# Optimization experiments

Measured on AMD Instinct MI355X. Metric: run time of the kernel, lower is better.

Reference implementation:

```python
import jax, jax.numpy as jnp
import numpy as np
import math

INF = 1e12  # constant.INFINITY_NUMBER in the original repo


def setup_inputs() -> dict:
    key = jax.random.key(0)
    ks = jax.random.split(key, 12)
    B, S, W, D = 16, 512, 8, 768
    M, Wm = 2, 64
    U, Wu = 32, 16
    V = 32000
    words = jax.random.randint(ks[0], (B, S, W), 0, V)
    masks = jax.random.randint(ks[1], (B, S, W), 0, 2).astype(bool)
    main = jax.random.randint(ks[2], (B, M, Wm), 0, V)
    main_mask = jax.random.randint(ks[3], (B, M, Wm), 0, 2).astype(bool)
    user = jax.random.randint(ks[4], (B, U, Wu), 0, V)
    user_mask = jax.random.randint(ks[5], (B, U, Wu), 0, 2).astype(bool)
    # sparse-ish dependency adjacency
    adj = (jax.random.uniform(ks[6], (B, S, S)) < 0.05).astype(jnp.float32)
    emb_weight = jax.random.normal(ks[7], (V, D), jnp.float32) * 0.02
    K_w = jax.random.normal(ks[8], (D, D), jnp.float32) * (1.0 / math.sqrt(D))
    K_b = jnp.zeros((D,), jnp.float32)
    Q_w = jax.random.normal(ks[9], (D, D), jnp.float32) * (1.0 / math.sqrt(D))
    Q_b = jnp.zeros((D,), jnp.float32)
    return {"words": words, "masks": masks, "main": main, "main_mask": main_mask,
            "user": user, "user_mask": user_mask, "adj": adj,
            "emb_weight": emb_weight, "K_w": K_w, "K_b": K_b, "Q_w": Q_w, "Q_b": Q_b}


def _masked_max(embs, mask, axis):
    # masked_fill(mask, -INF) -> max(axis) ; caller fixes residual -INF rows
    return jnp.max(jnp.where(mask[..., None], -INF, embs), axis=axis)


def reference(words, masks, main, main_mask, user, user_mask, adj,
              emb_weight, K_w, K_b, Q_w, Q_b):
    D = emb_weight.shape[1]

    word_embs = emb_weight[words]   # [B,S,W,D]
    main_embs = emb_weight[main]    # [B,M,Wm,D]
    user_embs = emb_weight[user]    # [B,U,Wu,D]

    # node mask from adjacency: True where node has no in/out edges
    mask = ((adj.sum(axis=2) + adj.sum(axis=1)) == 0)[:, :, None]  # [B,S,1]

    # main: masked max-pool over word pieces, zero fully-masked rows
    main_e = _masked_max(main_embs, main_mask, axis=2)             # [B,M,D]
    main_e = jnp.where(main_e == -INF, 0.0, main_e)

    # user: masked max-pool over word pieces then over users
    user_e = _masked_max(user_embs, user_mask, axis=2)             # [B,U,D]
    user_e = jnp.max(user_e, axis=1)                               # [B,D]
    user_e = jnp.where(user_e == -INF, 0.0, user_e)

    # token embeddings: masked max-pool over word pieces (no -INF fix in original)
    g = _masked_max(word_embs, masks, axis=2)                      # [B,S,D]

    # single-head attention: softmax(K g (Q g)^T / sqrt(D)) @ g
    key_ = g @ K_w.T + K_b                                         # [B,S,D]
    query = g @ Q_w.T + Q_b                                        # [B,S,D]
    scores = jnp.einsum('bsd,btd->bst', key_, query) / math.sqrt(D)
    dense_graph = jax.nn.softmax(scores, axis=2)                   # [B,S,S]
    gcn_out = jnp.einsum('bst,btd->bsd', dense_graph, g)           # [B,S,D]

    adj_sm = jax.nn.softmax(adj, axis=2)

    return (gcn_out, mask, dense_graph, adj_sm,
            jnp.squeeze(main_e), jnp.squeeze(user_e))
```

## Files before the change

kernel.cpp:

```cpp
#include <hip/hip_runtime.h>
#include <hip/hip_bf16.h>
#include <math.h>

static constexpr int Bn = 16, Sn = 512, Wn = 8, Dn = 768;
static constexpr int Mn_ = 2, WMn = 64;
static constexpr int Un = 32, WUn = 16;

#define INF_VAL 1e12f
#define INV_SQRT_D 0.03608439182435161f

static constexpr size_t OFF_GCN   = 0;
static constexpr size_t OFF_MASK  = 6291456;
static constexpr size_t OFF_DENSE = 6299648;
static constexpr size_t OFF_ADJ   = 10493952;
static constexpr size_t OFF_MAIN  = 14688256;
static constexpr size_t OFF_USER  = 14712832;

static constexpr size_t WSB_GBF     = 0;
static constexpr size_t WSB_GT      = 12582912;
static constexpr size_t WSB_DENSEBF = 25165824;
static constexpr size_t WSB_PARTU   = 33554432;
static constexpr size_t WSB_PARTM   = 35127296;
static constexpr size_t WSB_BCAT    = 35520512;
static constexpr size_t WSB_KBAR    = 35526656;
static constexpr size_t WSB_QBAR    = 35532800;
static constexpr size_t WSB_U       = 35538944;
static constexpr size_t WSB_V       = 35545088;
static constexpr size_t WSB_CONSTS  = 35551232;
static constexpr size_t WSB_QS      = 35551296;
static constexpr size_t WSB_KQ      = 35584064;
static constexpr size_t WSB_COLSUM  = 35616832;
static constexpr size_t WSB_FLAGS   = 35649600;
static constexpr size_t WSB_ROWSUM  = 35682368;
static constexpr size_t WSB_UVU     = 35715136;
static constexpr size_t WSB_UVV     = 35764288;

typedef __attribute__((ext_vector_type(8))) short short8;
typedef __attribute__((ext_vector_type(4))) float f32x4;

static __device__ __forceinline__ ushort f2bf(float f) {
    union { float f; unsigned u; } v; v.f = f;
    unsigned u = v.u;
    unsigned r = (u + 0x7FFFu + ((u >> 16) & 1u)) >> 16;
    return (ushort)r;
}

static __device__ __forceinline__ void gload16(const void* g, void* lds) {
    __builtin_amdgcn_global_load_lds(
        (const __attribute__((address_space(1))) void*)g,
        (__attribute__((address_space(3))) void*)lds, 16, 0, 0);
}

static __device__ __forceinline__ void fmax4(float4& a, const float4& x) {
    a.x = fmaxf(a.x, x.x); a.y = fmaxf(a.y, x.y);
    a.z = fmaxf(a.z, x.z); a.w = fmaxf(a.w, x.w);
}

__global__ __launch_bounds__(256)
void fold1(const float* __restrict__ K_w, const float* __restrict__ K_b,
           const float* __restrict__ Q_w, const float* __restrict__ Q_b,
           double* __restrict__ kbar, double* __restrict__ qbar,
           ushort* __restrict__ Kwb, ushort* __restrict__ Qwb,
           float* __restrict__ bcat, float* __restrict__ colsum) {
    int blk = blockIdx.x, t = threadIdx.x;
    if (blk < 192) {
        int wv = t >> 6, lane = t & 63;
        int r = blk * 4 + wv;
        double sk = 0.0, sq = 0.0;
        for (int d = lane; d < Dn; d += 64) {
            sk += (double)K_w[(size_t)r * Dn + d];
            sq += (double)Q_w[(size_t)r * Dn + d];
        }
        #pragma unroll
        for (int off = 32; off > 0; off >>= 1) {
            sk += __shfl_down(sk, off, 64);
            sq += __shfl_down(sq, off, 64);
        }
        if (lane == 0) {
            kbar[r] = -1e12 * sk + (double)K_b[r];
            qbar[r] = -1e12 * sq + (double)Q_b[r];
        }
    } else if (blk < 254) {
        const int NV = Dn * Dn / 4;
        for (int i = (blk - 192) * 256 + t; i < 2 * NV; i += 62 * 256) {
            float4 x; ushort4 o;
            if (i < NV) x = ((const float4*)K_w)[i];
            else        x = ((const float4*)Q_w)[i - NV];
            o.x = f2bf(x.x); o.y = f2bf(x.y); o.z = f2bf(x.z); o.w = f2bf(x.w);
            if (i < NV) ((ushort4*)Kwb)[i] = o;
            else        ((ushort4*)Qwb)[i - NV] = o;
        }
    } else if (blk == 254) {
        for (int i = t; i < 1536; i += 256)
            bcat[i] = (i < Dn) ? K_b[i] : Q_b[i - Dn];
    } else {
        for (int i = t; i < Bn * Sn; i += 256) colsum[i] = 0.f;
    }
}

__global__ __launch_bounds__(64)
void uv_part(const float* __restrict__ K_w, const float* __restrict__ Q_w,
             const double* __restrict__ kbar, const double* __restrict__ qbar,
             double* __restrict__ uvu, double* __restrict__ uvv) {
    int j = blockIdx.x * 64 + threadIdx.x;
    int e0 = blockIdx.y * 96;
    double su = 0.0, sv = 0.0;
    for (int e = e0; e < e0 + 96; ++e) {
        su += (double)K_w[(size_t)e * Dn + j] * qbar[e];
        sv += (double)Q_w[(size_t)e * Dn + j] * kbar[e];
    }
    uvu[(size_t)blockIdx.y * Dn + j] = su;
    uvv[(size_t)blockIdx.y * Dn + j] = sv;
}

__global__ __launch_bounds__(64)
void uvred_consts(const double* __restrict__ uvu, const double* __restrict__ uvv,
                  const double* __restrict__ kbar, const double* __restrict__ qbar,
                  const float* __restrict__ K_b, const float* __restrict__ Q_b,
                  double* __restrict__ u, double* __restrict__ v,
                  double* __restrict__ consts) {
    int blk = blockIdx.x;
    int l = threadIdx.x;
    if (blk < 12) {
        int j = blk * 64 + l;
        double su = 0.0, sv = 0.0;
        #pragma unroll
        for (int c = 0; c < 8; ++c) {
            su += uvu[(size_t)c * Dn + j];
            sv += uvv[(size_t)c * Dn + j];
        }
        u[j] = su; v[j] = sv;
    } else {
        double c0 = 0.0, c1 = 0.0, c2 = 0.0;
        for (int e = l; e < Dn; e += 64) {
            c0 += kbar[e] * (double)Q_b[e];
            c1 += kbar[e] * qbar[e];
            c2 += qbar[e] * (double)K_b[e];
        }
        #pragma unroll
        for (int off = 32; off > 0; off >>= 1) {
            c0 += __shfl_down(c0, off, 64);
            c1 += __shfl_down(c1, off, 64);
            c2 += __shfl_down(c2, off, 64);
        }
        if (l == 0) { consts[0] = c0; consts[1] = c1; consts[2] = c2; }
    }
}

__global__ __launch_bounds__(512)
void adjsm_colsum_kernel(const float* __restrict__ adj, float* __restrict__ adjsm,
                         float* __restrict__ colsum, float* __restrict__ rowsum) {
    int blk = blockIdx.x;
    int b = blk >> 5, rc = blk & 31;
    int t = threadIdx.x;
    const float* base = adj + ((size_t)b * Sn + rc * 16) * Sn;
    float* obase = adjsm + ((size_t)b * Sn + rc * 16) * Sn;
    const float EM1 = 0.36787944117144233f;
    const float EP1 = 2.718281828459045f;
    __shared__ float red[8];
    float colacc = 0.f;
    for (int r = 0; r < 16; ++r) {
        float a = base[(size_t)r * Sn + t];
        colacc += a;
        float s = a;
        #pragma unroll
        for (int off = 32; off > 0; off >>= 1) s += __shfl_down(s, off, 64);
        if ((t & 63) == 0) red[t >> 6] = s;
        __syncthreads();
        float n1 = red[0] + red[1] + red[2] + red[3]
                 + red[4] + red[5] + red[6] + red[7];
        float e1, e0;
        if (n1 > 0.f) { e1 = 1.f; e0 = EM1; } else { e1 = EP1; e0 = 1.f; }
        float denom = n1 * e1 + (512.f - n1) * e0;
        float inv = 1.f / denom;
        obase[(size_t)r * Sn + t] = (a == 1.f ? e1 : e0) * inv;
        if (t == 0) rowsum[(size_t)b * Sn + rc * 16 + r] = n1;
        __syncthreads();
    }
    atomicAdd(&colsum[(size_t)b * Sn + t], colacc);
}

__global__ __launch_bounds__(192)
void pool_g_kernel(const int* __restrict__ words, const int* __restrict__ masks,
                   const float* __restrict__ emb,
                   const double* __restrict__ u, const double* __restrict__ v,
                   const double* __restrict__ consts,
                   ushort* __restrict__ gbf, float* __restrict__ qs,
                   float* __restrict__ kq, int* __restrict__ flags) {
    int bs = blockIdx.x;
    int t = threadIdx.x;
    const int* wrow = words + (size_t)bs * Wn;
    const int* mrow = masks + (size_t)bs * Wn;
    float4 acc = make_float4(-INF_VAL, -INF_VAL, -INF_VAL, -INF_VAL);
    int nm = 0;
    #pragma unroll
    for (int w = 0; w < Wn; ++w) {
        int mk = mrow[w];
        nm += (mk != 0);
        if (mk != 0) continue;
        float4 x = ((const float4*)(emb + (size_t)wrow[w] * Dn))[t];
        fmax4(acc, x);
    }
    ushort4 o;
    o.x = f2bf(acc.x); o.y = f2bf(acc.y); o.z = f2bf(acc.z); o.w = f2bf(acc.w);
    ((ushort4*)(gbf + (size_t)bs * Dn))[t] = o;
    int j = t * 4;
    double dv = v[j] * (double)acc.x + v[j+1] * (double)acc.y
              + v[j+2] * (double)acc.z + v[j+3] * (double)acc.w;
    double du = u[j] * (double)acc.x + u[j+1] * (double)acc.y
              + u[j+2] * (double)acc.z + u[j+3] * (double)acc.w;
    #pragma unroll
    for (int off = 32; off > 0; off >>= 1) {
        dv += __shfl_down(dv, off, 64);
        du += __shfl_down(du, off, 64);
    }
    __shared__ double rr[6];
    if ((t & 63) == 0) { rr[t >> 6] = dv; rr[3 + (t >> 6)] = du; }
    __syncthreads();
    if (t == 0) {
        qs[bs] = (float)(rr[0] + rr[1] + rr[2] + consts[0]);
        kq[bs] = (float)(rr[3] + rr[4] + rr[5] + consts[2]);
        flags[bs] = (nm == Wn) ? 1 : 0;
    }
}

__global__ __launch_bounds__(192)
void pool_s1(const int* __restrict__ main_idx, const int* __restrict__ mmask,
             const int* __restrict__ user_idx, const int* __restrict__ umask,
             const float* __restrict__ emb,
             float* __restrict__ partM, float* __restrict__ partU) {
    int blk = blockIdx.x;
    int t = threadIdx.x;
    const int *irow, *mrow;
    float* dst;
    if (blk < 128) {
        int bm = blk >> 2, ch = blk & 3;
        irow = main_idx + (size_t)bm * WMn + ch * 16;
        mrow = mmask + (size_t)bm * WMn + ch * 16;
        dst = partM + (size_t)blk * Dn;
    } else {
        int bu = blk - 128;
        irow = user_idx + (size_t)bu * WUn;
        mrow = umask + (size_t)bu * WUn;
        dst = partU + (size_t)bu * Dn;
    }
    float4 acc = make_float4(-INF_VAL, -INF_VAL, -INF_VAL, -INF_VAL);
    #pragma unroll
    for (int w = 0; w < 16; ++w) {
        if (mrow[w] != 0) continue;
        float4 x = ((const float4*)(emb + (size_t)irow[w] * Dn))[t];
        fmax4(acc, x);
    }
    ((float4*)dst)[t] = acc;
}

__global__ __launch_bounds__(192)
void pool_s2m(const float* __restrict__ partM, const float* __restrict__ partU,
              float* __restrict__ outM, float* __restrict__ outU,
              const float* __restrict__ rowsum, const float* __restrict__ colsum,
              float* __restrict__ maskout) {
    int blk = blockIdx.x;
    int t = threadIdx.x;
    if (blk >= 48) {
        int i = (blk - 48) * 192 + t;
        if (i < Bn * Sn)
            maskout[i] = ((rowsum[i] + colsum[i]) == 0.f) ? 1.f : 0.f;
        return;
    }
    float4 acc = make_float4(-INF_VAL, -INF_VAL, -INF_VAL, -INF_VAL);
    float* dst;
    if (blk < 32) {
        #pragma unroll
        for (int c = 0; c < 4; ++c) {
            float4 x = ((const float4*)(partM + (size_t)(blk * 4 + c) * Dn))[t];
            fmax4(acc, x);
        }
        dst = outM + (size_t)blk * Dn;
    } else {
        int b = blk - 32;
        for (int u2 = 0; u2 < Un; ++u2) {
            float4 x = ((const float4*)(partU + (size_t)(b * Un + u2) * Dn))[t];
            fmax4(acc, x);
        }
        dst = outU + (size_t)b * Dn;
    }
    if (acc.x == -INF_VAL) acc.x = 0.f;
    if (acc.y == -INF_VAL) acc.y = 0.f;
    if (acc.z == -INF_VAL) acc.z = 0.f;
    if (acc.w == -INF_VAL) acc.w = 0.f;
    ((float4*)dst)[t] = acc;
}

__global__ __launch_bounds__(256)
void transpose_g(const ushort* __restrict__ gbf, ushort* __restrict__ gT) {
    __shared__ ushort tile[32][33];
    int b = blockIdx.z;
    int d0 = blockIdx.x * 32, s0 = blockIdx.y * 32;
    int tx = threadIdx.x & 31, ty = threadIdx.x >> 5;
    #pragma unroll
    for (int i = 0; i < 4; ++i)
        tile[ty + i * 8][tx] = gbf[((size_t)(b * Sn + s0 + ty + i * 8)) * Dn + d0 + tx];
    __syncthreads();
    #pragma unroll
    for (int i = 0; i < 4; ++i)
        gT[((size_t)(b * Dn + d0 + ty + i * 8)) * Sn + s0 + tx] = tile[tx][ty + i * 8];
}

template<int OUT_BF16, int HASBIAS, int SPLITC>
__global__ __launch_bounds__(256)
void gemm_mfma(const ushort* __restrict__ A, const ushort* __restrict__ B,
               const float* __restrict__ bias, void* __restrict__ Cout,
               void* __restrict__ Cout2,
               int Km, int lda, int ldb, int ldc,
               long long sA, long long sB, long long sC) {
    __shared__ ushort As[128 * 64];
    __shared__ ushort Bs[128 * 64];
    const ushort* Ab = A + (size_t)blockIdx.z * sA;
    const ushort* Bb = B + (size_t)blockIdx.z * sB;
    int i0 = blockIdx.y * 128, j0 = blockIdx.x * 128;
    int tid = threadIdx.x;
    int lane = tid & 63, wv = tid >> 6;
    int wr = wv >> 1, wc = wv & 1;
    int ln15 = lane & 15, lkg = lane >> 4;
    int sub = lane >> 3;
    int c8  = lane & 7;

    f32x4 acc[4][4] = {};

    for (int k0 = 0; k0 < Km; k0 += 64) {
        #pragma unroll
        for (int it = 0; it < 4; ++it) {
            int r = it * 32 + wv * 8 + sub;
            int cc = c8 ^ (r & 7);
            ushort* dstA = As + (it * 4096 + wv * 1024) / 2;
            ushort* dstB = Bs + (it * 4096 + wv * 1024) / 2;
            gload16(Ab + (size_t)(i0 + r) * lda + k0 + cc * 8, dstA);
            gload16(Bb + (size_t)(j0 + r) * ldb + k0 + cc * 8, dstB);
        }
        __syncthreads();
        #pragma unroll
        for (int kh = 0; kh < 2; ++kh) {
            short8 af[4], bfr[4];
            int kc = kh * 4 + lkg;
            #pragma unroll
            for (int f = 0; f < 4; ++f) {
                int ra = wr * 64 + f * 16 + ln15;
                af[f] = *(const short8*)((const char*)As + ra * 128 + ((kc ^ (ra & 7)) << 4));
                int rb = wc * 64 + f * 16 + ln15;
                bfr[f] = *(const short8*)((const char*)Bs + rb * 128 + ((kc ^ (rb & 7)) << 4));
            }
            #pragma unroll
            for (int fa = 0; fa < 4; ++fa)
                #pragma unroll
                for (int fb = 0; fb < 4; ++fb)
                    acc[fa][fb] = __builtin_amdgcn_mfma_f32_16x16x32_bf16(
                        af[fa], bfr[fb], acc[fa][fb], 0, 0, 0);
        }
        __syncthreads();
    }

    #pragma unroll
    for (int fa = 0; fa < 4; ++fa) {
        #pragma unroll
        for (int fb = 0; fb < 4; ++fb) {
            int n = j0 + wc * 64 + fb * 16 + ln15;
            float bv = HASBIAS ? bias[n] : 0.0f;
            #pragma unroll
            for (int rr = 0; rr < 4; ++rr) {
                int m = i0 + wr * 64 + fa * 16 + lkg * 4 + rr;
                float val = acc[fa][fb][rr] + bv;
                if (SPLITC) {
                    ushort* dst = (n < Dn) ? (ushort*)Cout : (ushort*)Cout2;
                    int nn = (n < Dn) ? n : n - Dn;
                    dst[(size_t)m * ldc + nn] = f2bf(val);
                } else if (OUT_BF16) {
                    ((ushort*)Cout)[(size_t)blockIdx.z * sC + (size_t)m * ldc + n] = f2bf(val);
                } else {
                    ((float*)Cout)[(size_t)blockIdx.z * sC + (size_t)m * ldc + n] = val;
                }
            }
        }
    }
}

__global__ __launch_bounds__(256)
void softmax_fix(float* __restrict__ dense, const int* __restrict__ flags,
                 const float* __restrict__ qs, const float* __restrict__ kq,
                 const double* __restrict__ consts, ushort* __restrict__ densebf) {
    int bs = blockIdx.x;
    int b = bs >> 9;
    int t = threadIdx.x;
    float* row = dense + (size_t)bs * 512;
    int f0 = flags[(b << 9) + t];
    int f1 = flags[(b << 9) + t + 256];
    bool sm = flags[bs] != 0;
    float x0, x1;
    if (sm) {
        float c1i = (float)consts[1] * INV_SQRT_D;
        x0 = f0 ? c1i : qs[(b << 9) + t] * INV_SQRT_D;
        x1 = f1 ? c1i : qs[(b << 9) + t + 256] * INV_SQRT_D;
    } else {
        float kqi = kq[bs] * INV_SQRT_D;
        x0 = f0 ? kqi : row[t] * INV_SQRT_D;
        x1 = f1 ? kqi : row[t + 256] * INV_SQRT_D;
    }
    float m = fmaxf(x0, x1);
    #pragma unroll
    for (int off = 32; off > 0; off >>= 1) m = fmaxf(m, __shfl_down(m, off, 64));
    __shared__ float red[4];
    __shared__ float bmax, bsum;
    if ((t & 63) == 0) red[t >> 6] = m;
    __syncthreads();
    if (t == 0) bmax = fmaxf(fmaxf(red[0], red[1]), fmaxf(red[2], red[3]));
    __syncthreads();
    float mx = bmax;
    float e0 = expf(x0 - mx), e1 = expf(x1 - mx);
    float s = e0 + e1;
    #pragma unroll
    for (int off = 32; off > 0; off >>= 1) s += __shfl_down(s, off, 64);
    if ((t & 63) == 0) red[t >> 6] = s;
    __syncthreads();
    if (t == 0) bsum = red[0] + red[1] + red[2] + red[3];
    __syncthreads();
    float inv = 1.f / bsum;
    float p0 = e0 * inv, p1 = e1 * inv;
    row[t] = p0; row[t + 256] = p1;
    ushort* bro = densebf + (size_t)bs * 512;
    bro[t] = f2bf(p0); bro[t + 256] = f2bf(p1);
}

extern "C" void kernel_launch(void* const* d_in, const int* in_sizes, int n_in,
                              void* d_out, int out_size, void* d_ws, size_t ws_size,
                              hipStream_t stream) {
    const int*   words     = (const int*)d_in[0];
    const int*   masks     = (const int*)d_in[1];
    const int*   main_idx  = (const int*)d_in[2];
    const int*   main_mask = (const int*)d_in[3];
    const int*   user_idx  = (const int*)d_in[4];
    const int*   user_mask = (const int*)d_in[5];
    const float* adj       = (const float*)d_in[6];
    const float* emb       = (const float*)d_in[7];
    const float* K_w       = (const float*)d_in[8];
    const float* K_b       = (const float*)d_in[9];
    const float* Q_w       = (const float*)d_in[10];
    const float* Q_b       = (const float*)d_in[11];

    float* out = (float*)d_out;
    char*  ws8 = (char*)d_ws;

    ushort* gbf     = (ushort*)(ws8 + WSB_GBF);
    ushort* gT      = (ushort*)(ws8 + WSB_GT);
    ushort* densebf = (ushort*)(ws8 + WSB_DENSEBF);
    float*  partU   = (float*)(ws8 + WSB_PARTU);
    float*  partM   = (float*)(ws8 + WSB_PARTM);
    float*  bcat    = (float*)(ws8 + WSB_BCAT);
    double* kbar    = (double*)(ws8 + WSB_KBAR);
    double* qbar    = (double*)(ws8 + WSB_QBAR);
    double* u       = (double*)(ws8 + WSB_U);
    double* v       = (double*)(ws8 + WSB_V);
    double* consts  = (double*)(ws8 + WSB_CONSTS);
    float*  qs      = (float*)(ws8 + WSB_QS);
    float*  kq      = (float*)(ws8 + WSB_KQ);
    float*  colsum  = (float*)(ws8 + WSB_COLSUM);
    int*    flags   = (int*)(ws8 + WSB_FLAGS);
    float*  rowsum  = (float*)(ws8 + WSB_ROWSUM);
    double* uvu     = (double*)(ws8 + WSB_UVU);
    double* uvv     = (double*)(ws8 + WSB_UVV);

    ushort* Kwb     = (ushort*)(out + OFF_DENSE);
    ushort* Qwb     = Kwb + (size_t)Dn * Dn;
    ushort* keybf   = (ushort*)(out + OFF_GCN);
    ushort* querybf = keybf + (size_t)Bn * Sn * Dn;
    float*  dense   = out + OFF_DENSE;

    fold1<<<256, 256, 0, stream>>>(K_w, K_b, Q_w, Q_b, kbar, qbar, Kwb, Qwb, bcat, colsum);
    uv_part<<<dim3(Dn / 64, 8), 64, 0, stream>>>(K_w, Q_w, kbar, qbar, uvu, uvv);
    uvred_consts<<<13, 64, 0, stream>>>(uvu, uvv, kbar, qbar, K_b, Q_b, u, v, consts);

    adjsm_colsum_kernel<<<Bn * 32, 512, 0, stream>>>(adj, out + OFF_ADJ, colsum, rowsum);

    pool_g_kernel<<<Bn * Sn, 192, 0, stream>>>(words, masks, emb, u, v, consts,
                                               gbf, qs, kq, flags);
    pool_s1<<<640, 192, 0, stream>>>(main_idx, main_mask, user_idx, user_mask,
                                     emb, partM, partU);
    pool_s2m<<<91, 192, 0, stream>>>(partM, partU, out + OFF_MAIN, out + OFF_USER,
                                     rowsum, colsum, out + OFF_MASK);

    transpose_g<<<dim3(Dn / 32, Sn / 32, Bn), 256, 0, stream>>>(gbf, gT);

    gemm_mfma<1, 1, 1><<<dim3(2 * Dn / 128, (Bn * Sn) / 128, 1), 256, 0, stream>>>(
        gbf, Kwb, bcat, keybf, querybf, Dn, Dn, Dn, Dn, 0, 0, 0);

    gemm_mfma<0, 0, 0><<<dim3(Sn / 128, Sn / 128, Bn), 256, 0, stream>>>(
        keybf, querybf, nullptr, dense, nullptr, Dn, Dn, Dn, Sn,
        (long long)Sn * Dn, (long long)Sn * Dn, (long long)Sn * Sn);

    softmax_fix<<<Bn * Sn, 256, 0, stream>>>(dense, flags, qs, kq, consts, densebf);

    gemm_mfma<0, 0, 0><<<dim3(Dn / 128, Sn / 128, Bn), 256, 0, stream>>>(
        densebf, gT, nullptr, out + OFF_GCN, nullptr, Sn, Sn, Sn, Dn,
        (long long)Sn * Sn, (long long)Dn * Sn, (long long)Sn * Dn);
}
```

Measured before the change: 170.4 us.

## Fold K and Q projections into a single precomputed D×D matrix

The attention scores are reassociated as g·(K_wᵀQ_w)·gᵀ. A D×D product matrix Mt is computed once, then a single GEMM g·Mt gives h. The previous path used two projection GEMMs producing key and query. Bias cross-terms become per-row and per-column scalar corrections (ga, gb, consts[3]) that the softmax kernel adds. This halves the projection GEMM work, at the cost of an extra small weight transpose and GEMM, and bf16 rounding of the folded matrix may shift numerics.

```diff
diff --git a/kernel.cpp b/kernel.cpp
--- a/kernel.cpp
+++ b/kernel.cpp
@@ -19,21 +19,30 @@
 static constexpr size_t WSB_GBF     = 0;
 static constexpr size_t WSB_GT      = 12582912;
 static constexpr size_t WSB_DENSEBF = 25165824;
-static constexpr size_t WSB_PARTU   = 33554432;
-static constexpr size_t WSB_PARTM   = 35127296;
-static constexpr size_t WSB_BCAT    = 35520512;
-static constexpr size_t WSB_KBAR    = 35526656;
-static constexpr size_t WSB_QBAR    = 35532800;
-static constexpr size_t WSB_U       = 35538944;
-static constexpr size_t WSB_V       = 35545088;
-static constexpr size_t WSB_CONSTS  = 35551232;
-static constexpr size_t WSB_QS      = 35551296;
-static constexpr size_t WSB_KQ      = 35584064;
-static constexpr size_t WSB_COLSUM  = 35616832;
-static constexpr size_t WSB_FLAGS   = 35649600;
-static constexpr size_t WSB_ROWSUM  = 35682368;
-static constexpr size_t WSB_UVU     = 35715136;
-static constexpr size_t WSB_UVV     = 35764288;
+static constexpr size_t WSB_HBF     = 33554432;
+static constexpr size_t WSB_KWT     = 46137344;
+static constexpr size_t WSB_QWT     = 47316992;
+static constexpr size_t WSB_MT      = 48496640;
+static constexpr size_t WSB_PARTU   = 49676288;
+static constexpr size_t WSB_PARTM   = 51249152;
+static constexpr size_t WSB_KBAR    = 51642368;
+static constexpr size_t WSB_QBAR    = 51648512;
+static constexpr size_t WSB_U       = 51654656;
+static constexpr size_t WSB_V       = 51660800;
+static constexpr size_t WSB_VA      = 51666944;
+static constexpr size_t WSB_VB      = 51673088;
+static constexpr size_t WSB_CONSTS  = 51679232;
+static constexpr size_t WSB_QS      = 51679296;
+static constexpr size_t WSB_KQ      = 51712064;
+static constexpr size_t WSB_GA      = 51744832;
+static constexpr size_t WSB_GB      = 51777600;
+static constexpr size_t WSB_COLSUM  = 51810368;
+static constexpr size_t WSB_FLAGS   = 51843136;
+static constexpr size_t WSB_ROWSUM  = 51875904;
+static constexpr size_t WSB_UVU     = 51908672;
+static constexpr size_t WSB_UVV     = 51957824;
+static constexpr size_t WSB_UVA     = 52006976;
+static constexpr size_t WSB_UVB     = 52056128;
 
 typedef __attribute__((ext_vector_type(8))) short short8;
 typedef __attribute__((ext_vector_type(4))) float f32x4;
@@ -60,8 +69,8 @@
 void fold1(const float* __restrict__ K_w, const float* __restrict__ K_b,
            const float* __restrict__ Q_w, const float* __restrict__ Q_b,
            double* __restrict__ kbar, double* __restrict__ qbar,
-           ushort* __restrict__ Kwb, ushort* __restrict__ Qwb,
-           float* __restrict__ bcat, float* __restrict__ colsum) {
+           ushort* __restrict__ KwbT, ushort* __restrict__ QwbT,
+           float* __restrict__ colsum) {
     int blk = blockIdx.x, t = threadIdx.x;
     if (blk < 192) {
         int wv = t >> 6, lane = t & 63;
@@ -80,19 +89,21 @@
             kbar[r] = -1e12 * sk + (double)K_b[r];
             qbar[r] = -1e12 * sq + (double)Q_b[r];
         }
-    } else if (blk < 254) {
-        const int NV = Dn * Dn / 4;
-        for (int i = (blk - 192) * 256 + t; i < 2 * NV; i += 62 * 256) {
-            float4 x; ushort4 o;
-            if (i < NV) x = ((const float4*)K_w)[i];
-            else        x = ((const float4*)Q_w)[i - NV];
-            o.x = f2bf(x.x); o.y = f2bf(x.y); o.z = f2bf(x.z); o.w = f2bf(x.w);
-            if (i < NV) ((ushort4*)Kwb)[i] = o;
-            else        ((ushort4*)Qwb)[i - NV] = o;
-        }
-    } else if (blk == 254) {
-        for (int i = t; i < 1536; i += 256)
-            bcat[i] = (i < Dn) ? K_b[i] : Q_b[i - Dn];
+    } else if (blk < 1344) {
+        int tt = blk - 192;
+        const float* src = (tt < 576) ? K_w : Q_w;
+        ushort* dst = (tt < 576) ? KwbT : QwbT;
+        int t6 = (tt < 576) ? tt : tt - 576;
+        int e0 = (t6 % 24) * 32, i0 = (t6 / 24) * 32;
+        __shared__ ushort tile[32][33];
+        int tx = t & 31, ty = t >> 5;
+        #pragma unroll
+        for (int i2 = 0; i2 < 4; ++i2)
+            tile[ty + i2 * 8][tx] = f2bf(src[(size_t)(e0 + ty + i2 * 8) * Dn + i0 + tx]);
+        __syncthreads();
+        #pragma unroll
+        for (int i2 = 0; i2 < 4; ++i2)
+            dst[(size_t)(i0 + ty + i2 * 8) * Dn + e0 + tx] = tile[tx][ty + i2 * 8];
     } else {
         for (int i = t; i < Bn * Sn; i += 256) colsum[i] = 0.f;
     }
@@ -100,50 +111,64 @@
 
 __global__ __launch_bounds__(64)
 void uv_part(const float* __restrict__ K_w, const float* __restrict__ Q_w,
+             const float* __restrict__ K_b, const float* __restrict__ Q_b,
              const double* __restrict__ kbar, const double* __restrict__ qbar,
-             double* __restrict__ uvu, double* __restrict__ uvv) {
+             double* __restrict__ uvu, double* __restrict__ uvv,
+             double* __restrict__ uva, double* __restrict__ uvb) {
     int j = blockIdx.x * 64 + threadIdx.x;
     int e0 = blockIdx.y * 96;
-    double su = 0.0, sv = 0.0;
+    double su = 0.0, sv = 0.0, sa = 0.0, sb = 0.0;
     for (int e = e0; e < e0 + 96; ++e) {
-        su += (double)K_w[(size_t)e * Dn + j] * qbar[e];
-        sv += (double)Q_w[(size_t)e * Dn + j] * kbar[e];
+        double kw = (double)K_w[(size_t)e * Dn + j];
+        double qw = (double)Q_w[(size_t)e * Dn + j];
+        su += kw * qbar[e];
+        sv += qw * kbar[e];
+        sa += kw * (double)Q_b[e];
+        sb += qw * (double)K_b[e];
     }
     uvu[(size_t)blockIdx.y * Dn + j] = su;
     uvv[(size_t)blockIdx.y * Dn + j] = sv;
+    uva[(size_t)blockIdx.y * Dn + j] = sa;
+    uvb[(size_t)blockIdx.y * Dn + j] = sb;
 }
 
 __global__ __launch_bounds__(64)
 void uvred_consts(const double* __restrict__ uvu, const double* __restrict__ uvv,
+                  const double* __restrict__ uva, const double* __restrict__ uvb,
                   const double* __restrict__ kbar, const double* __restrict__ qbar,
                   const float* __restrict__ K_b, const float* __restrict__ Q_b,
                   double* __restrict__ u, double* __restrict__ v,
+                  double* __restrict__ va, double* __restrict__ vb,
                   double* __restrict__ consts) {
     int blk = blockIdx.x;
     int l = threadIdx.x;
     if (blk < 12) {
         int j = blk * 64 + l;
-        double su = 0.0, sv = 0.0;
+        double su = 0.0, sv = 0.0, sa = 0.0, sb = 0.0;
         #pragma unroll
         for (int c = 0; c < 8; ++c) {
             su += uvu[(size_t)c * Dn + j];
             sv += uvv[(size_t)c * Dn + j];
-        }
-        u[j] = su; v[j] = sv;
+            sa += uva[(size_t)c * Dn + j];
+            sb += uvb[(size_t)c * Dn + j];
+        }
+        u[j] = su; v[j] = sv; va[j] = sa; vb[j] = sb;
     } else {
-        double c0 = 0.0, c1 = 0.0, c2 = 0.0;
+        double c0 = 0.0, c1 = 0.0, c2 = 0.0, c3 = 0.0;
         for (int e = l; e < Dn; e += 64) {
             c0 += kbar[e] * (double)Q_b[e];
             c1 += kbar[e] * qbar[e];
             c2 += qbar[e] * (double)K_b[e];
+            c3 += (double)K_b[e] * (double)Q_b[e];
         }
         #pragma unroll
         for (int off = 32; off > 0; off >>= 1) {
             c0 += __shfl_down(c0, off, 64);
             c1 += __shfl_down(c1, off, 64);
             c2 += __shfl_down(c2, off, 64);
-        }
-        if (l == 0) { consts[0] = c0; consts[1] = c1; consts[2] = c2; }
+            c3 += __shfl_down(c3, off, 64);
+        }
+        if (l == 0) { consts[0] = c0; consts[1] = c1; consts[2] = c2; consts[3] = c3; }
     }
 }
 
@@ -184,9 +209,11 @@
 void pool_g_kernel(const int* __restrict__ words, const int* __restrict__ masks,
                    const float* __restrict__ emb,
                    const double* __restrict__ u, const double* __restrict__ v,
+                   const double* __restrict__ va, const double* __restrict__ vb,
                    const double* __restrict__ consts,
                    ushort* __restrict__ gbf, float* __restrict__ qs,
-                   float* __restrict__ kq, int* __restrict__ flags) {
+                   float* __restrict__ kq, float* __restrict__ ga,
+                   float* __restrict__ gb, int* __restrict__ flags) {
     int bs = blockIdx.x;
     int t = threadIdx.x;
     const int* wrow = words + (size_t)bs * Wn;
@@ -209,17 +236,28 @@
               + v[j+2] * (double)acc.z + v[j+3] * (double)acc.w;
     double du = u[j] * (double)acc.x + u[j+1] * (double)acc.y
               + u[j+2] * (double)acc.z + u[j+3] * (double)acc.w;
+    double da = va[j] * (double)acc.x + va[j+1] * (double)acc.y
+              + va[j+2] * (double)acc.z + va[j+3] * (double)acc.w;
+    double db = vb[j] * (double)acc.x + vb[j+1] * (double)acc.y
+              + vb[j+2] * (double)acc.z + vb[j+3] * (double)acc.w;
     #pragma unroll
     for (int off = 32; off > 0; off >>= 1) {
         dv += __shfl_down(dv, off, 64);
         du += __shfl_down(du, off, 64);
-    }
-    __shared__ double rr[6];
-    if ((t & 63) == 0) { rr[t >> 6] = dv; rr[3 + (t >> 6)] = du; }
+        da += __shfl_down(da, off, 64);
+        db += __shfl_down(db, off, 64);
+    }
+    __shared__ double rr[12];
+    if ((t & 63) == 0) {
+        rr[t >> 6] = dv; rr[3 + (t >> 6)] = du;
+        rr[6 + (t >> 6)] = da; rr[9 + (t >> 6)] = db;
+    }
     __syncthreads();
     if (t == 0) {
         qs[bs] = (float)(rr[0] + rr[1] + rr[2] + consts[0]);
         kq[bs] = (float)(rr[3] + rr[4] + rr[5] + consts[2]);
+        ga[bs] = (float)(rr[6] + rr[7] + rr[8]);
+        gb[bs] = (float)(rr[9] + rr[10] + rr[11]);
         flags[bs] = (nm == Wn) ? 1 : 0;
     }
 }
@@ -306,11 +344,10 @@
         gT[((size_t)(b * Dn + d0 + ty + i * 8)) * Sn + s0 + tx] = tile[tx][ty + i * 8];
 }
 
-template<int OUT_BF16, int HASBIAS, int SPLITC>
+template<int OUT_BF16>
 __global__ __launch_bounds__(256)
 void gemm_mfma(const ushort* __restrict__ A, const ushort* __restrict__ B,
-               const float* __restrict__ bias, void* __restrict__ Cout,
-               void* __restrict__ Cout2,
+               void* __restrict__ Cout,
                int Km, int lda, int ldb, int ldc,
                long long sA, long long sB, long long sC) {
     __shared__ ushort As[128 * 64];
@@ -364,16 +401,11 @@
         #pragma unroll
         for (int fb = 0; fb < 4; ++fb) {
             int n = j0 + wc * 64 + fb * 16 + ln15;
-            float bv = HASBIAS ? bias[n] : 0.0f;
             #pragma unroll
             for (int rr = 0; rr < 4; ++rr) {
                 int m = i0 + wr * 64 + fa * 16 + lkg * 4 + rr;
-                float val = acc[fa][fb][rr] + bv;
-                if (SPLITC) {
-                    ushort* dst = (n < Dn) ? (ushort*)Cout : (ushort*)Cout2;
-                    int nn = (n < Dn) ? n : n - Dn;
-                    dst[(size_t)m * ldc + nn] = f2bf(val);
-                } else if (OUT_BF16) {
+                float val = acc[fa][fb][rr];
+                if (OUT_BF16) {
                     ((ushort*)Cout)[(size_t)blockIdx.z * sC + (size_t)m * ldc + n] = f2bf(val);
                 } else {
                     ((float*)Cout)[(size_t)blockIdx.z * sC + (size_t)m * ldc + n] = val;
@@ -386,6 +418,7 @@
 __global__ __launch_bounds__(256)
 void softmax_fix(float* __restrict__ dense, const int* __restrict__ flags,
                  const float* __restrict__ qs, const float* __restrict__ kq,
+                 const float* __restrict__ ga, const float* __restrict__ gb,
                  const double* __restrict__ consts, ushort* __restrict__ densebf) {
     int bs = blockIdx.x;
     int b = bs >> 9;
@@ -401,8 +434,9 @@
         x1 = f1 ? c1i : qs[(b << 9) + t + 256] * INV_SQRT_D;
     } else {
         float kqi = kq[bs] * INV_SQRT_D;
-        x0 = f0 ? kqi : row[t] * INV_SQRT_D;
-        x1 = f1 ? kqi : row[t + 256] * INV_SQRT_D;
+        float corr = ga[bs] + (float)consts[3];
+        x0 = f0 ? kqi : (row[t] + corr + gb[(b << 9) + t]) * INV_SQRT_D;
+        x1 = f1 ? kqi : (row[t + 256] + corr + gb[(b << 9) + t + 256]) * INV_SQRT_D;
     }
     float m = fmaxf(x0, x1);
     #pragma unroll
@@ -451,36 +485,46 @@
     ushort* gbf     = (ushort*)(ws8 + WSB_GBF);
     ushort* gT      = (ushort*)(ws8 + WSB_GT);
     ushort* densebf = (ushort*)(ws8 + WSB_DENSEBF);
+    ushort* hbf     = (ushort*)(ws8 + WSB_HBF);
+    ushort* KwbT    = (ushort*)(ws8 + WSB_KWT);
+    ushort* QwbT    = (ushort*)(ws8 + WSB_QWT);
+    ushort* Mt      = (ushort*)(ws8 + WSB_MT);
     float*  partU   = (float*)(ws8 + WSB_PARTU);
     float*  partM   = (float*)(ws8 + WSB_PARTM);
-    float*  bcat    = (float*)(ws8 + WSB_BCAT);
     double* kbar    = (double*)(ws8 + WSB_KBAR);
     double* qbar    = (double*)(ws8 + WSB_QBAR);
     double* u       = (double*)(ws8 + WSB_U);
     double* v       = (double*)(ws8 + WSB_V);
+    double* va      = (double*)(ws8 + WSB_VA);
+    double* vb      = (double*)(ws8 + WSB_VB);
     double* consts  = (double*)(ws8 + WSB_CONSTS);
     float*  qs      = (float*)(ws8 + WSB_QS);
     float*  kq      = (float*)(ws8 + WSB_KQ);
+    float*  ga      = (float*)(ws8 + WSB_GA);
+    float*  gb      = (float*)(ws8 + WSB_GB);
     float*  colsum  = (float*)(ws8 + WSB_COLSUM);
     int*    flags   = (int*)(ws8 + WSB_FLAGS);
     float*  rowsum  = (float*)(ws8 + WSB_ROWSUM);
     double* uvu     = (double*)(ws8 + WSB_UVU);
     double* uvv     = (double*)(ws8 + WSB_UVV);
-
-    ushort* Kwb     = (ushort*)(out + OFF_DENSE);
-    ushort* Qwb     = Kwb + (size_t)Dn * Dn;
-    ushort* keybf   = (ushort*)(out + OFF_GCN);
-    ushort* querybf = keybf + (size_t)Bn * Sn * Dn;
-    float*  dense   = out + OFF_DENSE;
-
-    fold1<<<256, 256, 0, stream>>>(K_w, K_b, Q_w, Q_b, kbar, qbar, Kwb, Qwb, bcat, colsum);
-    uv_part<<<dim3(Dn / 64, 8), 64, 0, stream>>>(K_w, Q_w, kbar, qbar, uvu, uvv);
-    uvred_consts<<<13, 64, 0, stream>>>(uvu, uvv, kbar, qbar, K_b, Q_b, u, v, consts);
+    double* uva     = (double*)(ws8 + WSB_UVA);
+    double* uvb     = (double*)(ws8 + WSB_UVB);
+
+    float* dense = out + OFF_DENSE;
+
+    fold1<<<1345, 256, 0, stream>>>(K_w, K_b, Q_w, Q_b, kbar, qbar, KwbT, QwbT, colsum);
+    uv_part<<<dim3(Dn / 64, 8), 64, 0, stream>>>(K_w, Q_w, K_b, Q_b, kbar, qbar,
+                                                 uvu, uvv, uva, uvb);
+    uvred_consts<<<13, 64, 0, stream>>>(uvu, uvv, uva, uvb, kbar, qbar, K_b, Q_b,
+                                        u, v, va, vb, consts);
+
+    gemm_mfma<1><<<dim3(6, 6, 1), 256, 0, stream>>>(
+        QwbT, KwbT, Mt, Dn, Dn, Dn, Dn, 0, 0, 0);
 
     adjsm_colsum_kernel<<<Bn * 32, 512, 0, stream>>>(adj, out + OFF_ADJ, colsum, rowsum);
 
-    pool_g_kernel<<<Bn * Sn, 192, 0, stream>>>(words, masks, emb, u, v, consts,
-                                               gbf, qs, kq, flags);
+    pool_g_kernel<<<Bn * Sn, 192, 0, stream>>>(words, masks, emb, u, v, va, vb, consts,
+                                               gbf, qs, kq, ga, gb, flags);
     pool_s1<<<640, 192, 0, stream>>>(main_idx, main_mask, user_idx, user_mask,
                                      emb, partM, partU);
     pool_s2m<<<91, 192, 0, stream>>>(partM, partU, out + OFF_MAIN, out + OFF_USER,
@@ -488,16 +532,16 @@
 
     transpose_g<<<dim3(Dn / 32, Sn / 32, Bn), 256, 0, stream>>>(gbf, gT);
 
-    gemm_mfma<1, 1, 1><<<dim3(2 * Dn / 128, (Bn * Sn) / 128, 1), 256, 0, stream>>>(
-        gbf, Kwb, bcat, keybf, querybf, Dn, Dn, Dn, Dn, 0, 0, 0);
-
-    gemm_mfma<0, 0, 0><<<dim3(Sn / 128, Sn / 128, Bn), 256, 0, stream>>>(
-        keybf, querybf, nullptr, dense, nullptr, Dn, Dn, Dn, Sn,
+    gemm_mfma<1><<<dim3(6, 64, 1), 256, 0, stream>>>(
+        gbf, Mt, hbf, Dn, Dn, Dn, Dn, 0, 0, 0);
+
+    gemm_mfma<0><<<dim3(4, 4, Bn), 256, 0, stream>>>(
+        hbf, gbf, dense, Dn, Dn, Dn, Sn,
         (long long)Sn * Dn, (long long)Sn * Dn, (long long)Sn * Sn);
 
-    softmax_fix<<<Bn * Sn, 256, 0, stream>>>(dense, flags, qs, kq, consts, densebf);
-
-    gemm_mfma<0, 0, 0><<<dim3(Dn / 128, Sn / 128, Bn), 256, 0, stream>>>(
-        densebf, gT, nullptr, out + OFF_GCN, nullptr, Sn, Sn, Sn, Dn,
+    softmax_fix<<<Bn * Sn, 256, 0, stream>>>(dense, flags, qs, kq, ga, gb, consts, densebf);
+
+    gemm_mfma<0><<<dim3(6, 4, Bn), 256, 0, stream>>>(
+        densebf, gT, out + OFF_GCN, Sn, Sn, Sn, Dn,
         (long long)Sn * Sn, (long long)Dn * Sn, (long long)Sn * Dn);
 }
```

Result: no change. 171.7 us (+0.8%).
